# Kernel tuning notes

Hardware: AMD Instinct MI355X
Metric: run time of the kernel (lower is better)

## Reference

```python
import jax, jax.numpy as jnp
import numpy as np

B, G, A = 16, 50, 81920          # batch, max_gt_num, anchor_num
T, P = 128, 64                   # train_anchors_num, max positives (T*positive_ratios)
NNEG = T - P                     # max negatives per image
BIG = 1e10


def setup_inputs():
    key = jax.random.key(0)
    k1, k2, k3, k4, k5, k6, k7 = jax.random.split(key, 7)
    # anchors: CTPN-style, fixed width 16, heights ~[11, 273]
    ay1 = jax.random.uniform(k1, (B, A)) * 960.0
    ax1 = jax.random.uniform(k2, (B, A)) * 1000.0
    ah = jax.random.uniform(k3, (B, A)) * 262.0 + 11.0
    anchors = jnp.stack([ay1, ax1, ay1 + ah, ax1 + 16.0], axis=-1)
    # gt boxes: 30 valid per image, rest padding (tag=0)
    gy1 = jax.random.uniform(k4, (B, G)) * 900.0
    gx1 = jax.random.uniform(k5, (B, G)) * 600.0
    gh = jax.random.uniform(k6, (B, G)) * 180.0 + 20.0
    gw = jax.random.uniform(k7, (B, G)) * 380.0 + 16.0
    tag = jnp.broadcast_to((jnp.arange(G) < 30).astype(jnp.float32), (B, G))
    boxes = jnp.stack([gy1, gx1, gy1 + gh, gx1 + gw], axis=-1) * tag[..., None]
    gt_boxes = jnp.concatenate([boxes, tag[..., None]], axis=-1)       # [B,G,5]
    gt_cls = jnp.stack([tag, tag], axis=-1)                            # [B,G,2] (class_id, tag)
    valid_anchors_indices = jnp.broadcast_to(jnp.arange(A, dtype=jnp.int32), (B, A))
    return {"gt_boxes": gt_boxes, "gt_cls": gt_cls, "anchors": anchors,
            "valid_anchors_indices": valid_anchors_indices}


def _compute_iou(gb, an):
    # gb [G,4], an [A,4] -> [G,A]
    iw = jnp.maximum(0.0, jnp.minimum(gb[:, None, 3], an[None, :, 3]) -
                     jnp.maximum(gb[:, None, 1], an[None, :, 1]))
    ih = jnp.maximum(0.0, jnp.minimum(gb[:, None, 2], an[None, :, 2]) -
                     jnp.maximum(gb[:, None, 0], an[None, :, 0]))
    inter = iw * ih
    area_g = (gb[:, 3] - gb[:, 1]) * (gb[:, 2] - gb[:, 0])
    area_a = (an[:, 3] - an[:, 1]) * (an[:, 2] - an[:, 0])
    return inter / (area_g[:, None] + area_a[None, :] - inter)


def _one_image(gt_boxes, gt_cls, anchors, valid_idx, key):
    gt_tag = gt_boxes[:, 4] > 0                       # [G] padding mask
    gb = gt_boxes[:, :4]
    gcls = gt_cls[:, 0]
    gt_num = jnp.sum(gt_tag.astype(jnp.float32))

    iou = _compute_iou(gb, anchors) * gt_tag[:, None].astype(jnp.float32)   # [G,A]
    gt_max_bool = (iou == jnp.max(iou, axis=1, keepdims=True)) & gt_tag[:, None]
    a_max = jnp.max(iou, axis=0, keepdims=True)
    a_thr = jnp.where(a_max >= 0.7, a_max, 1.0)
    pos_mat = (gt_max_bool | (iou == a_thr)) & gt_tag[:, None]              # [G,A]

    k1, k2 = jax.random.split(key)
    # --- positive sampling (random shuffle -> random-score top_k) ---
    flat = pos_mat.reshape(-1)
    score = jnp.where(flat, jax.random.uniform(k1, (G * A,)), -1.0)
    top_s, top_i = jax.lax.top_k(score, P)
    pos_valid = top_s >= 0.0                                               # [P]
    pos_num = jnp.sum(pos_valid.astype(jnp.int32))
    gt_i = top_i // A
    a_i = top_i % A
    pa = anchors[a_i]
    pg = gb[gt_i]
    pc = gcls[gt_i] * pos_valid
    h = pa[:, 2] - pa[:, 0]
    gt_h = jnp.where(pos_valid, pg[:, 2] - pg[:, 0], h)   # safe for padding slots
    dy = ((pg[:, 2] + pg[:, 0]) - (pa[:, 2] + pa[:, 0])) * 0.5 / h
    dh = jnp.log(gt_h / h)
    pd = jnp.stack([dy / 0.1, dh / 0.2], axis=1) * pos_valid[:, None]       # [P,2]

    # --- side anchors per gt ---
    x1b = jnp.broadcast_to(anchors[:, 1][None, :], (G, A))
    left_i = jnp.argmin(jnp.where(pos_mat, x1b, BIG), axis=1)
    right_i = jnp.argmax(jnp.where(pos_mat, x1b, -BIG), axis=1)
    la, ra = anchors[left_i], anchors[right_i]
    ld = (gb[:, 1] - (la[:, 3] + la[:, 1]) * 0.5) / (la[:, 3] - la[:, 1]) / 0.1
    rd = (gb[:, 3] - (ra[:, 3] + ra[:, 1]) * 0.5) / (ra[:, 3] - ra[:, 1]) / 0.1
    gtf = gt_tag.astype(jnp.float32)
    side_deltas = jnp.stack([ld * gtf, rd * gtf, gtf], axis=1)              # [G,3]
    gti = gt_tag.astype(jnp.int32)
    side_indices = jnp.stack([valid_idx[left_i] * gti, valid_idx[right_i] * gti, gti], axis=1)

    # --- negative sampling ---
    neg_bool = (jnp.max(iou, axis=0) < 0.5) & ~jnp.any(pos_mat, axis=0)
    nscore = jnp.where(neg_bool, jax.random.uniform(k2, (A,)), -1.0)
    ns, ni = jax.lax.top_k(nscore, NNEG)
    neg_avail = jnp.sum((ns >= 0.0).astype(jnp.int32))
    neg_num = jnp.minimum(jnp.minimum(NNEG, T - pos_num), neg_avail)

    # --- fixed-size assembly: slots [0,pos_num)=pos, [pos_num,pos_num+neg_num)=neg ---
    i = jnp.arange(T)
    is_pos = i < pos_num
    is_neg = (i >= pos_num) & (i < pos_num + neg_num)
    pi = jnp.clip(i, 0, P - 1)
    nj = jnp.clip(i - pos_num, 0, NNEG - 1)
    tagc = (is_pos | is_neg).astype(jnp.float32)
    deltas = jnp.concatenate([jnp.where(is_pos[:, None], pd[pi], 0.0), tagc[:, None]], axis=1)
    class_ids = jnp.stack([jnp.where(is_pos, pc[pi], 0.0), tagc], axis=1)
    idx_pos = valid_idx[a_i]                                                # [P]
    ind = jnp.where(is_pos, idx_pos[pi],
                    jnp.where(is_neg, ni[nj].astype(jnp.int32), 0))
    ind_tag = jnp.where(is_pos, 1, jnp.where(is_neg, -1, 0)).astype(jnp.int32)
    indices = jnp.stack([ind, ind_tag], axis=1)

    return (deltas, class_ids, indices, side_deltas, side_indices,
            gt_num, pos_num.astype(jnp.float32), neg_num.astype(jnp.float32))


def reference(gt_boxes, gt_cls, anchors, valid_anchors_indices):
    keys = jax.random.split(jax.random.key(42), B)
    return jax.vmap(_one_image)(gt_boxes, gt_cls, anchors, valid_anchors_indices, keys)
```

## Files before the change

### kernel.cpp

```cpp
#include <hip/hip_runtime.h>
#include <stdint.h>

namespace ct {
constexpr int B = 16, G = 50, A = 81920, T = 128;
constexpr int NB2 = 64;
constexpr int CH2 = A / (NB2 * 256);
constexpr int CAPP = 16384;
constexpr int CAPN = 16384;
constexpr int STG  = 2048;
constexpr int NX = 16, NY = 20, NCELL = NX * NY;
constexpr float NEG_T1 = 0.992f;

constexpr size_t O_DELTAS = 0;
constexpr size_t O_CLS = O_DELTAS + (size_t)B * T * 3;
constexpr size_t O_IND = O_CLS + (size_t)B * T * 2;
constexpr size_t O_SD  = O_IND + (size_t)B * T * 2;
constexpr size_t O_SI  = O_SD + (size_t)B * G * 3;
constexpr size_t O_GTN = O_SI + (size_t)B * G * 3;
constexpr size_t O_PN  = O_GTN + B;
constexpr size_t O_NN  = O_PN + B;

constexpr size_t W_LEFT  = 0;
constexpr size_t W_GTMAX = 8192;
constexpr size_t W_RIGHT = 11392;
constexpr size_t W_CPOS  = 17792;
constexpr size_t W_CT1   = 18816;
constexpr size_t W_ZERO0 = W_GTMAX;
constexpr size_t W_ZSIZE = 19840 - W_GTMAX;
constexpr size_t W_BCNT  = 19840;
constexpr size_t W_POSL  = 24064;
constexpr size_t W_NT1   = W_POSL + 8ull * B * CAPP;
}

struct U2 { uint32_t x, y; };

__device__ __forceinline__ U2 threefry(uint32_t k0, uint32_t k1, uint32_t x0, uint32_t x1) {
  uint32_t ks2 = k0 ^ k1 ^ 0x1BD11BDAu;
  x0 += k0; x1 += k1;
#define TFR(r) { x0 += x1; x1 = (x1 << (r)) | (x1 >> (32 - (r))); x1 ^= x0; }
  TFR(13) TFR(15) TFR(26) TFR(6)  x0 += k1;  x1 += ks2 + 1u;
  TFR(17) TFR(29) TFR(16) TFR(24) x0 += ks2; x1 += k0 + 2u;
  TFR(13) TFR(15) TFR(26) TFR(6)  x0 += k0;  x1 += k1 + 3u;
  TFR(17) TFR(29) TFR(16) TFR(24) x0 += k1;  x1 += ks2 + 4u;
  TFR(13) TFR(15) TFR(26) TFR(6)  x0 += ks2; x1 += k0 + 5u;
#undef TFR
  return {x0, x1};
}

__device__ __forceinline__ uint32_t rnd_bits(uint32_t ka, uint32_t kb, uint32_t idx) {
  U2 o = threefry(ka, kb, 0u, idx);
  return o.x ^ o.y;
}

__device__ __forceinline__ void iou_parts(float g0, float g1, float g2, float g3,
                                          float garea,
                                          float a0, float a1, float a2, float a3,
                                          float aarea, float& inter, float& denom) {
#pragma clang fp contract(off)
  float iw = fminf(g3, a3) - fmaxf(g1, a1);
  iw = fmaxf(0.0f, iw);
  float ih = fminf(g2, a2) - fmaxf(g0, a0);
  ih = fmaxf(0.0f, ih);
  inter = iw * ih;
  denom = (garea + aarea) - inter;
}

__device__ __forceinline__ void compact_gts(const float* gt_boxes, int b, int tid,
                                            float4* sgA, float* sgG, int* sgO,
                                            int* sn) {
  using namespace ct;
  int lane = tid & 63;
  if (tid < 64) {
    bool pred = false;
    float g0 = 0, g1 = 0, g2 = 0, g3 = 0;
    if (tid < G) {
      const float* gp = gt_boxes + ((size_t)b * G + tid) * 5;
      g0 = gp[0]; g1 = gp[1]; g2 = gp[2]; g3 = gp[3];
      pred = gp[4] > 0.0f;
    }
    unsigned long long mk = __ballot(pred);
    int slot = (int)__popcll(mk & ((1ull << lane) - 1ull));
    if (pred) {
      sgA[slot] = make_float4(g0, g1, g2, g3);
      sgG[slot] = (g3 - g1) * (g2 - g0);
      sgO[slot] = tid;
    }
    if (lane == 0) *sn = (int)__popcll(mk);
  }
}

__device__ __forceinline__ void build_cellmask(const float4* sgA, int ntag, int tid,
                                               unsigned long long* sCM) {
  using namespace ct;
  for (int c = tid; c < NCELL; c += 256) {
    int cx = c & (NX - 1), cy = c >> 4;
    float x0 = cx * 64.0f, x1 = x0 + 64.0f;
    float y0 = cy * 64.0f, y1 = y0 + 64.0f;
    unsigned long long m = 0;
    for (int j = 0; j < ntag; ++j) {
      float4 g = sgA[j];
      if (g.y < x1 && g.w > x0 && g.x < y1 && g.z > y0) m |= 1ull << j;
    }
    sCM[c] = m;
  }
}

__device__ __forceinline__ unsigned long long anchor_mask(const unsigned long long* sCM,
                                                          float4 an) {
  using namespace ct;
  int cx0 = min((int)an.y >> 6, NX - 1), cx1 = min((int)an.w >> 6, NX - 1);
  int cy0 = min((int)an.x >> 6, NY - 1), cy1 = min((int)an.z >> 6, NY - 1);
  unsigned long long mask = 0;
  for (int cy = cy0; cy <= cy1; ++cy)
    for (int cx = cx0; cx <= cx1; ++cx)
      mask |= sCM[cy * NX + cx];
  return mask;
}

__global__ __launch_bounds__(256) void k1b_gtmax(const float* __restrict__ anchors,
                                                 const float* __restrict__ gt_boxes,
                                                 char* ws) {
  using namespace ct;
  __shared__ float4 sgA[64];
  __shared__ float  sgG[64];
  __shared__ int    sgO[64];
  __shared__ int    sn;
  __shared__ uint32_t sGm[64];
  __shared__ unsigned long long sCM[NCELL];
  int b = blockIdx.y, tid = threadIdx.x;
  compact_gts(gt_boxes, b, tid, sgA, sgG, sgO, &sn);
  if (tid < 64) sGm[tid] = 0u;
  __syncthreads();
  build_cellmask(sgA, sn, tid, sCM);
  __syncthreads();
  const float4* ap = (const float4*)(anchors + (size_t)b * A * 4);
  for (int c = 0; c < CH2; ++c) {
    int a = (blockIdx.x * CH2 + c) * 256 + tid;
    float4 an = ap[a];
    float aarea = (an.w - an.y) * (an.z - an.x);
    unsigned long long mask = anchor_mask(sCM, an);
    while (mask) {
      int j = (int)(__ffsll((long long)mask) - 1);
      mask &= mask - 1;
      float4 g = sgA[j];
      float inter, denom;
      iou_parts(g.x, g.y, g.z, g.w, sgG[j], an.x, an.y, an.z, an.w, aarea, inter, denom);
      float v = inter / denom;
      if (v > 0.0f) atomicMax(&sGm[j], __float_as_uint(v));
    }
  }
  __syncthreads();
  if (tid < sn && sGm[tid] != 0u)
    atomicMax((uint32_t*)(ws + W_GTMAX) + (size_t)b * G + sgO[tid], sGm[tid]);
}

__global__ __launch_bounds__(256) void k2_posneg(const float* __restrict__ anchors,
                                                 const float* __restrict__ gt_boxes,
                                                 char* ws) {
  using namespace ct;
  __shared__ float4 sgA[64];
  __shared__ float  sgG[64];
  __shared__ int    sgO[64];
  __shared__ float  sgM[64];
  __shared__ int    sn;
  __shared__ unsigned long long sCM[NCELL];
  __shared__ uint32_t sK[4];
  __shared__ uint32_t sT1C[CH2];
  __shared__ uint32_t sWT1[CH2][4];
  __shared__ uint32_t sPfx[CH2];
  __shared__ uint32_t sNegW[4];
  __shared__ uint32_t sT1Base;
  int b = blockIdx.y, tid = threadIdx.x, lane = tid & 63, wid = tid >> 6;
  compact_gts(gt_boxes, b, tid, sgA, sgG, sgO, &sn);
  if (tid < CH2) sT1C[tid] = 0u;
  if (tid == 64 || (tid == 0 && blockDim.x == 64)) {}
  if (tid == 65 % 256) {}
  if (tid == 66 % 256) {}
  if (tid == 0) {
    U2 kb = threefry(0u, 42u, 0u, (uint32_t)b);
    U2 s0 = threefry(kb.x, kb.y, 0u, 0u);
    U2 s1 = threefry(kb.x, kb.y, 0u, 1u);
    sK[0] = s0.x; sK[1] = s0.y;
    sK[2] = s1.x; sK[3] = s1.y;
  }
  __syncthreads();
  build_cellmask(sgA, sn, tid, sCM);
  __syncthreads();
  if (tid < sn)
    sgM[tid] = __uint_as_float(((const uint32_t*)(ws + W_GTMAX))[(size_t)b * G + sgO[tid]]);
  __syncthreads();

  uint32_t k1a = sK[0], k1b = sK[1], k2a = sK[2], k2b = sK[3];
  unsigned long long* posl  = (unsigned long long*)(ws + W_POSL) + (size_t)b * CAPP;
  unsigned long long* negt1 = (unsigned long long*)(ws + W_NT1)  + (size_t)b * CAPN;
  unsigned long long* left  = (unsigned long long*)(ws + W_LEFT)  + (size_t)b * G;
  unsigned long long* right = (unsigned long long*)(ws + W_RIGHT) + (size_t)b * G;
  const float4* ap = (const float4*)(anchors + (size_t)b * A * 4);

  unsigned long long nkv[CH2];
  uint32_t offv[CH2];
  bool t1v[CH2];
  uint32_t negAcc = 0;

  for (int c = 0; c < CH2; ++c) {
    int a = (blockIdx.x * CH2 + c) * 256 + tid;
    float4 an = ap[a];
    float aarea = (an.w - an.y) * (an.z - an.x);
    unsigned long long mask = anchor_mask(sCM, an);

    float amax = 0.0f;
    unsigned long long mEq = 0, mMax = 0;
    unsigned long long t0 = mask;
    while (t0) {
      int j = (int)(__ffsll((long long)t0) - 1);
      t0 &= t0 - 1;
      float4 g = sgA[j];
      float inter, denom;
      iou_parts(g.x, g.y, g.z, g.w, sgG[j], an.x, an.y, an.z, an.w, aarea, inter, denom);
      float v = inter / denom;
      mEq |= (v == sgM[j]) ? (1ull << j) : 0ull;
      if (v > amax) { amax = v; mMax = 1ull << j; }
      else mMax |= (v == amax) ? (1ull << j) : 0ull;
    }
    unsigned long long pm = mEq | (amax >= 0.7f ? mMax : 0ull);

    if (__ballot(pm != 0)) {
      unsigned long long t = pm;
      while (t) {
        int j = (int)(__ffsll((long long)t) - 1);
        t &= t - 1;
        int g = sgO[j];
        uint32_t jg = (uint32_t)g * (uint32_t)A + (uint32_t)a;
        uint32_t m = rnd_bits(k1a, k1b, jg) >> 9;
        unsigned long long pk = ((unsigned long long)(m + 1u) << 32) | (0xFFFFFFFFu - jg);
        uint32_t idx = atomicAdd((uint32_t*)(ws + W_CPOS) + b * 16, 1u);
        if (idx < (uint32_t)CAPP) posl[idx] = pk;
        unsigned long long x1b = (unsigned long long)__float_as_uint(an.y);
        atomicMin(left + g,  (x1b << 32) | (uint32_t)a);
        atomicMax(right + g, (x1b << 32) | (0xFFFFFFFFu - (uint32_t)a));
      }
    }

    bool isneg = (amax < 0.5f) && (pm == 0);
    uint32_t m2 = rnd_bits(k2a, k2b, (uint32_t)a) >> 9;
    nkv[c] = ((unsigned long long)(m2 + 1u) << 32) | (0xFFFFFFFFu - (uint32_t)a);
    t1v[c] = isneg && ((float)m2 * (1.0f / 8388608.0f) >= NEG_T1);
    unsigned long long nm = __ballot(isneg);
    unsigned long long tm = __ballot(t1v[c]);
    offv[c] = (uint32_t)__popcll(tm & ((1ull << lane) - 1ull));
    if (lane == 0) {
      negAcc += (uint32_t)__popcll(nm);
      sWT1[c][wid] = atomicAdd(&sT1C[c], (uint32_t)__popcll(tm));
    }
  }
  if (lane == 0) sNegW[wid] = negAcc;
  __syncthreads();
  if (tid == 0) {
    uint32_t tot = 0;
    for (int c = 0; c < CH2; ++c) { sPfx[c] = tot; tot += sT1C[c]; }
    sT1Base = tot ? atomicAdd((uint32_t*)(ws + W_CT1) + b * 16, tot) : 0u;
    ((uint32_t*)(ws + W_BCNT))[b * NB2 + blockIdx.x] =
        sNegW[0] + sNegW[1] + sNegW[2] + sNegW[3];
  }
  __syncthreads();
  uint32_t base = sT1Base;
  for (int c = 0; c < CH2; ++c) {
    if (t1v[c]) {
      uint32_t idx = base + sPfx[c] + sWT1[c][wid] + offv[c];
      if (idx < (uint32_t)CAPN) negt1[idx] = nkv[c];
    }
  }
}

__device__ void select_top64(const unsigned long long* gsrc, int n,
                             unsigned long long* stage, unsigned long long* sel,
                             unsigned long long* wmax) {
  using namespace ct;
  int tid = threadIdx.x, lane = tid & 63, wid = tid >> 6;
  const unsigned long long* p = gsrc;
  if (n <= STG) {
    for (int i = tid; i < n; i += 256) stage[i] = gsrc[i];
    p = stage;
  }
  __syncthreads();
  unsigned long long prev = ~0ull;
  for (int k = 0; k < 64; ++k) {
    unsigned long long lm = 0;
    for (int i = tid; i < n; i += 256) {
      unsigned long long v = p[i];
      if (v < prev && v > lm) lm = v;
    }
#pragma unroll
    for (int off = 32; off >= 1; off >>= 1) {
      unsigned long long o = __shfl_xor(lm, off, 64);
      if (o > lm) lm = o;
    }
    if (lane == 0) wmax[wid] = lm;
    __syncthreads();
    if (tid == 0) {
      unsigned long long m = wmax[0];
      for (int w = 1; w < 4; ++w) if (wmax[w] > m) m = wmax[w];
      sel[k] = m;
    }
    __syncthreads();
    prev = sel[k];
  }
}

__device__ void bitonic_desc(const unsigned long long* gsrc, int n,
                             unsigned long long* stage) {
  int tid = threadIdx.x;
  int sz = 64;
  while (sz < n) sz <<= 1;
  for (int i = tid; i < sz; i += 256) stage[i] = (i < n) ? gsrc[i] : 0ull;
  __syncthreads();
  for (int k = 2; k <= sz; k <<= 1) {
    for (int j = k >> 1; j > 0; j >>= 1) {
      for (int i = tid; i < sz; i += 256) {
        int l = i ^ j;
        if (l > i) {
          unsigned long long a = stage[i], c = stage[l];
          bool dir = (i & k) == 0;
          if ((a < c) == dir) { stage[i] = c; stage[l] = a; }
        }
      }
      __syncthreads();
    }
  }
}

__global__ __launch_bounds__(256) void k345_out(const float* __restrict__ anchors,
                                                const float* __restrict__ gt_boxes,
                                                const float* __restrict__ gt_cls,
                                                const int* __restrict__ vidx,
                                                char* ws, float* __restrict__ out) {
  using namespace ct;
  __shared__ unsigned long long stage[STG];
  __shared__ unsigned long long sel[64];
  __shared__ unsigned long long wmax[4];
  __shared__ uint32_t scnt[4];
  __shared__ float sPD0[64], sPD1[64], sPC[64], sIPF[64];
  __shared__ int sNI[64];
  __shared__ int sPn, sNn;
  int b = blockIdx.x, tid = threadIdx.x, lane = tid & 63, wid = tid >> 6;

  {
    int n = (int)min(((const uint32_t*)(ws + W_CPOS))[b * 16], (uint32_t)CAPP);
    const unsigned long long* src = (const unsigned long long*)(ws + W_POSL) + (size_t)b * CAPP;
    if (n <= STG) {
      bitonic_desc(src, n, stage);
      if (tid < 64) sel[tid] = stage[tid];
      __syncthreads();
    } else {
      select_top64(src, n, stage, sel, wmax);
    }
    int npos = n < 64 ? n : 64;
    if (tid == 0) sPn = npos;
    if (tid < 64) {
      float pd0 = 0.0f, pd1 = 0.0f, pcv = 0.0f, ipf = 0.0f;
      if (tid < npos) {
        uint32_t j = 0xFFFFFFFFu - (uint32_t)sel[tid];
        int g = j / (uint32_t)A, a = j % (uint32_t)A;
        const float* gp = gt_boxes + ((size_t)b * G + g) * 5;
        float4 an = *(const float4*)(anchors + ((size_t)b * A + a) * 4);
        float h = an.z - an.x;
        float gt_h = gp[2] - gp[0];
        float dy = (gp[2] + gp[0] - (an.z + an.x)) * 0.5f / h;
        float dh = logf(gt_h / h);
        pd0 = dy / 0.1f;
        pd1 = dh / 0.2f;
        pcv = gt_cls[((size_t)b * G + g) * 2];
        ipf = (float)vidx[(size_t)b * A + a];
      }
      sPD0[tid] = pd0; sPD1[tid] = pd1; sPC[tid] = pcv; sIPF[tid] = ipf;
    }
  }
  __syncthreads();

  {
    const uint32_t* bc = (const uint32_t*)(ws + W_BCNT) + (size_t)b * NB2;
    uint32_t callv = 0;
    for (int i = tid; i < NB2; i += 256) callv += bc[i];
#pragma unroll
    for (int off = 32; off >= 1; off >>= 1) callv += __shfl_xor(callv, off, 64);
    if (lane == 0) scnt[wid] = callv;
    __syncthreads();
    int call = (int)(scnt[0] + scnt[1] + scnt[2] + scnt[3]);
    int c1 = (int)min(((const uint32_t*)(ws + W_CT1))[b * 16], (uint32_t)CAPN);
    if (c1 <= STG) {
      bitonic_desc((const unsigned long long*)(ws + W_NT1) + (size_t)b * CAPN, c1, stage);
      if (tid < 64) sel[tid] = stage[tid];
      __syncthreads();
    } else {
      select_top64((const unsigned long long*)(ws + W_NT1) + (size_t)b * CAPN, c1,
                   stage, sel, wmax);
    }
    int nn = call < 64 ? call : 64;
    if (nn > c1) nn = c1;
    if (tid == 0) sNn = nn;
    if (tid < 64) {
      int v = 0;
      if (tid < nn) v = (int)(0xFFFFFFFFu - (uint32_t)sel[tid]);
      sNI[tid] = v;
    }
  }
  __syncthreads();

  int pn = sPn, nn = sNn;
  if (tid < T) {
    int t = tid;
    bool ispos = t < pn;
    bool isneg = (t >= pn) && (t < pn + nn);
    float tagc = (ispos || isneg) ? 1.0f : 0.0f;
    int tp = t < 63 ? t : 63;
    float d0 = ispos ? sPD0[tp] : 0.0f;
    float d1 = ispos ? sPD1[tp] : 0.0f;
    out[O_DELTAS + ((size_t)b * T + t) * 3 + 0] = d0;
    out[O_DELTAS + ((size_t)b * T + t) * 3 + 1] = d1;
    out[O_DELTAS + ((size_t)b * T + t) * 3 + 2] = tagc;
    out[O_CLS + ((size_t)b * T + t) * 2 + 0] = ispos ? sPC[tp] : 0.0f;
    out[O_CLS + ((size_t)b * T + t) * 2 + 1] = tagc;
    float iv = 0.0f, itag = 0.0f;
    if (ispos) { iv = sIPF[tp]; itag = 1.0f; }
    else if (isneg) {
      int nj = t - pn; nj = nj < 63 ? nj : 63;
      iv = (float)sNI[nj]; itag = -1.0f;
    }
    out[O_IND + ((size_t)b * T + t) * 2 + 0] = iv;
    out[O_IND + ((size_t)b * T + t) * 2 + 1] = itag;
  }
  if (tid >= 128 && tid < 128 + G) {
    int g = tid - 128;
    const float* gp = gt_boxes + ((size_t)b * G + g) * 5;
    float tag = gp[4] > 0.0f ? 1.0f : 0.0f;
    float sd0 = 0.0f, sd1 = 0.0f, si0 = 0.0f, si1 = 0.0f;
    if (tag > 0.0f) {
      unsigned long long lp = ((const unsigned long long*)(ws + W_LEFT))[(size_t)b * G + g];
      unsigned long long rp = ((const unsigned long long*)(ws + W_RIGHT))[(size_t)b * G + g];
      int al = (int)(uint32_t)lp;
      int ar = (int)(0xFFFFFFFFu - (uint32_t)rp);
      float4 la = *(const float4*)(anchors + ((size_t)b * A + al) * 4);
      float4 ra = *(const float4*)(anchors + ((size_t)b * A + ar) * 4);
      sd0 = (gp[1] - (la.w + la.y) * 0.5f) / (la.w - la.y) / 0.1f;
      sd1 = (gp[3] - (ra.w + ra.y) * 0.5f) / (ra.w - ra.y) / 0.1f;
      si0 = (float)vidx[(size_t)b * A + al];
      si1 = (float)vidx[(size_t)b * A + ar];
    }
    out[O_SD + ((size_t)b * G + g) * 3 + 0] = sd0;
    out[O_SD + ((size_t)b * G + g) * 3 + 1] = sd1;
    out[O_SD + ((size_t)b * G + g) * 3 + 2] = tag;
    out[O_SI + ((size_t)b * G + g) * 3 + 0] = si0;
    out[O_SI + ((size_t)b * G + g) * 3 + 1] = si1;
    out[O_SI + ((size_t)b * G + g) * 3 + 2] = tag;
  }
  if (tid == 190) {
    float s = 0.0f;
    for (int g = 0; g < G; ++g)
      s += (gt_boxes[((size_t)b * G + g) * 5 + 4] > 0.0f) ? 1.0f : 0.0f;
    out[O_GTN + b] = s;
  }
  if (tid == 191) out[O_PN + b] = (float)pn;
  if (tid == 192) out[O_NN + b] = (float)nn;
}

extern "C" void kernel_launch(void* const* d_in, const int* in_sizes, int n_in,
                              void* d_out, int out_size, void* d_ws, size_t ws_size,
                              hipStream_t stream) {
  using namespace ct;
  (void)in_sizes; (void)n_in; (void)out_size; (void)ws_size;
  const float* gt_boxes = (const float*)d_in[0];
  const float* gt_cls   = (const float*)d_in[1];
  const float* anchors  = (const float*)d_in[2];
  const int*   vidx     = (const int*)d_in[3];
  float* out = (float*)d_out;
  char* ws = (char*)d_ws;

  hipMemsetAsync(ws + W_LEFT, 0xFF, 8ull * B * G, stream);
  hipMemsetAsync(ws + W_ZERO0, 0, W_ZSIZE, stream);
  k1b_gtmax<<<dim3(NB2, B), dim3(256), 0, stream>>>(anchors, gt_boxes, ws);
  k2_posneg<<<dim3(NB2, B), dim3(256), 0, stream>>>(anchors, gt_boxes, ws);
  k345_out<<<dim3(B), dim3(256), 0, stream>>>(anchors, gt_boxes, gt_cls, vidx, ws, out);
}
```

Before: 178.4 us.

## Replace workspace memsets with init kernel precomputing cell masks and RNG keys

Adds an init kernel, one block per image, that replaces the two hipMemsetAsync calls by clearing only the workspace entries that are needed. The same kernel builds the per-image grid cell → gt bitmask table and the threefry subkeys once, in global memory. The two anchor-scanning kernels now copy the cell-mask table into shared memory and read the keys, instead of rebuilding them in each of their 1024 blocks. This trades redundant per-block setup and one extra launch for a small global read. The narrower zeroing (e.g., the counter region is no longer cleared) is a correctness risk if anything relied on the old memset.

```diff
diff --git a/kernel.cpp b/kernel.cpp
--- a/kernel.cpp
+++ b/kernel.cpp
@@ -20,16 +20,16 @@
 constexpr size_t O_PN  = O_GTN + B;
 constexpr size_t O_NN  = O_PN + B;
 
-constexpr size_t W_LEFT  = 0;
-constexpr size_t W_GTMAX = 8192;
-constexpr size_t W_RIGHT = 11392;
-constexpr size_t W_CPOS  = 17792;
-constexpr size_t W_CT1   = 18816;
-constexpr size_t W_ZERO0 = W_GTMAX;
-constexpr size_t W_ZSIZE = 19840 - W_GTMAX;
-constexpr size_t W_BCNT  = 19840;
+constexpr size_t W_KEYS  = 0;
+constexpr size_t W_GTMAX = 256;
+constexpr size_t W_LEFT  = 4096;
+constexpr size_t W_RIGHT = 10496;
+constexpr size_t W_CPOS  = 17408;
+constexpr size_t W_CT1   = 18432;
+constexpr size_t W_BCNT  = 19584;
 constexpr size_t W_POSL  = 24064;
 constexpr size_t W_NT1   = W_POSL + 8ull * B * CAPP;
+constexpr size_t W_CMASK = W_NT1  + 8ull * B * CAPN;
 }
 
 struct U2 { uint32_t x, y; };
@@ -89,9 +89,34 @@
   }
 }
 
-__device__ __forceinline__ void build_cellmask(const float4* sgA, int ntag, int tid,
-                                               unsigned long long* sCM) {
-  using namespace ct;
+__global__ __launch_bounds__(256) void k01_init(const float* __restrict__ gt_boxes,
+                                                char* ws) {
+  using namespace ct;
+  __shared__ float4 sgA[64];
+  __shared__ float  sgG[64];
+  __shared__ int    sgO[64];
+  __shared__ int    sn;
+  int b = blockIdx.x, tid = threadIdx.x;
+  if (tid == 0) {
+    uint32_t* keys = (uint32_t*)(ws + W_KEYS);
+    U2 kb = threefry(0u, 42u, 0u, (uint32_t)b);
+    U2 s0 = threefry(kb.x, kb.y, 0u, 0u);
+    U2 s1 = threefry(kb.x, kb.y, 0u, 1u);
+    keys[b * 4 + 0] = s0.x; keys[b * 4 + 1] = s0.y;
+    keys[b * 4 + 2] = s1.x; keys[b * 4 + 3] = s1.y;
+    ((uint32_t*)(ws + W_CPOS))[b * 16] = 0u;
+    ((uint32_t*)(ws + W_CT1))[b * 16] = 0u;
+  }
+  if (tid >= 64 && tid < 64 + G) {
+    int i = tid - 64;
+    ((unsigned long long*)(ws + W_LEFT))[(size_t)b * G + i] = ~0ull;
+    ((unsigned long long*)(ws + W_RIGHT))[(size_t)b * G + i] = 0ull;
+    ((uint32_t*)(ws + W_GTMAX))[(size_t)b * G + i] = 0u;
+  }
+  compact_gts(gt_boxes, b, tid, sgA, sgG, sgO, &sn);
+  __syncthreads();
+  int ntag = sn;
+  unsigned long long* cm = (unsigned long long*)(ws + W_CMASK) + (size_t)b * NCELL;
   for (int c = tid; c < NCELL; c += 256) {
     int cx = c & (NX - 1), cy = c >> 4;
     float x0 = cx * 64.0f, x1 = x0 + 64.0f;
@@ -101,7 +126,7 @@
       float4 g = sgA[j];
       if (g.y < x1 && g.w > x0 && g.x < y1 && g.z > y0) m |= 1ull << j;
     }
-    sCM[c] = m;
+    cm[c] = m;
   }
 }
 
@@ -130,8 +155,8 @@
   int b = blockIdx.y, tid = threadIdx.x;
   compact_gts(gt_boxes, b, tid, sgA, sgG, sgO, &sn);
   if (tid < 64) sGm[tid] = 0u;
-  __syncthreads();
-  build_cellmask(sgA, sn, tid, sCM);
+  const unsigned long long* cm = (const unsigned long long*)(ws + W_CMASK) + (size_t)b * NCELL;
+  for (int c = tid; c < NCELL; c += 256) sCM[c] = cm[c];
   __syncthreads();
   const float4* ap = (const float4*)(anchors + (size_t)b * A * 4);
   for (int c = 0; c < CH2; ++c) {
@@ -164,7 +189,6 @@
   __shared__ float  sgM[64];
   __shared__ int    sn;
   __shared__ unsigned long long sCM[NCELL];
-  __shared__ uint32_t sK[4];
   __shared__ uint32_t sT1C[CH2];
   __shared__ uint32_t sWT1[CH2][4];
   __shared__ uint32_t sPfx[CH2];
@@ -173,24 +197,16 @@
   int b = blockIdx.y, tid = threadIdx.x, lane = tid & 63, wid = tid >> 6;
   compact_gts(gt_boxes, b, tid, sgA, sgG, sgO, &sn);
   if (tid < CH2) sT1C[tid] = 0u;
-  if (tid == 64 || (tid == 0 && blockDim.x == 64)) {}
-  if (tid == 65 % 256) {}
-  if (tid == 66 % 256) {}
-  if (tid == 0) {
-    U2 kb = threefry(0u, 42u, 0u, (uint32_t)b);
-    U2 s0 = threefry(kb.x, kb.y, 0u, 0u);
-    U2 s1 = threefry(kb.x, kb.y, 0u, 1u);
-    sK[0] = s0.x; sK[1] = s0.y;
-    sK[2] = s1.x; sK[3] = s1.y;
-  }
-  __syncthreads();
-  build_cellmask(sgA, sn, tid, sCM);
+  const unsigned long long* cm = (const unsigned long long*)(ws + W_CMASK) + (size_t)b * NCELL;
+  for (int c = tid; c < NCELL; c += 256) sCM[c] = cm[c];
   __syncthreads();
   if (tid < sn)
     sgM[tid] = __uint_as_float(((const uint32_t*)(ws + W_GTMAX))[(size_t)b * G + sgO[tid]]);
   __syncthreads();
 
-  uint32_t k1a = sK[0], k1b = sK[1], k2a = sK[2], k2b = sK[3];
+  const uint32_t* keys = (const uint32_t*)(ws + W_KEYS);
+  uint32_t k1a = keys[b * 4 + 0], k1b = keys[b * 4 + 1];
+  uint32_t k2a = keys[b * 4 + 2], k2b = keys[b * 4 + 3];
   unsigned long long* posl  = (unsigned long long*)(ws + W_POSL) + (size_t)b * CAPP;
   unsigned long long* negt1 = (unsigned long long*)(ws + W_NT1)  + (size_t)b * CAPN;
   unsigned long long* left  = (unsigned long long*)(ws + W_LEFT)  + (size_t)b * G;
@@ -475,8 +491,7 @@
   float* out = (float*)d_out;
   char* ws = (char*)d_ws;
 
-  hipMemsetAsync(ws + W_LEFT, 0xFF, 8ull * B * G, stream);
-  hipMemsetAsync(ws + W_ZERO0, 0, W_ZSIZE, stream);
+  k01_init<<<dim3(B), dim3(256), 0, stream>>>(gt_boxes, ws);
   k1b_gtmax<<<dim3(NB2, B), dim3(256), 0, stream>>>(anchors, gt_boxes, ws);
   k2_posneg<<<dim3(NB2, B), dim3(256), 0, stream>>>(anchors, gt_boxes, ws);
   k345_out<<<dim3(B), dim3(256), 0, stream>>>(anchors, gt_boxes, gt_cls, vidx, ws, out);
```

After: 167.5 us. -6.1%, faster.
